# Kernel optimization log

Measured on AMD Instinct MI355X. Metric: run time of the kernel, lower is better.

## Reference

```python
import jax, jax.numpy as jnp
import numpy as np

NEG = -1e6  # SequenceMask fill value from original code


def setup_inputs() -> dict:
    key = jax.random.key(0)
    ks = jax.random.split(key, 7)
    B, Tq, Tk, U = 32, 1024, 1024, 256
    return {
        "query": jax.random.normal(ks[0], (B, Tq, U), dtype=jnp.float32),
        "key": jax.random.normal(ks[1], (B, Tk, U), dtype=jnp.float32),
        "value": jax.random.normal(ks[2], (B, Tk, U), dtype=jnp.float32),
        "valid_length": jax.random.randint(ks[3], (B,), 0, Tk, dtype=jnp.int32),
        "W_k": jax.random.normal(ks[4], (U, U), dtype=jnp.float32) * (1.0 / np.sqrt(U)),
        "W_q": jax.random.normal(ks[5], (U, U), dtype=jnp.float32) * (1.0 / np.sqrt(U)),
        "v": jax.random.normal(ks[6], (U,), dtype=jnp.float32) * (1.0 / np.sqrt(U)),
    }


def reference(query, key, value, valid_length, W_k, W_q, v):
    # Original applies W_k to query and W_q to key (naming swap kept faithfully).
    tq = jnp.tanh(jnp.einsum('bqu,vu->bqv', query, W_k))  # (B,Tq,U)
    tk = jnp.tanh(jnp.einsum('bku,vu->bkv', key, W_q))    # (B,Tk,U)
    # v is linear over (tq_i + tk_j): decompose to avoid (B,Tq,Tk,U) tensor.
    sq = jnp.einsum('bqu,u->bq', tq, v)  # (B,Tq)
    sk = jnp.einsum('bku,u->bk', tk, v)  # (B,Tk)
    scores = sq[:, :, None] + sk[:, None, :]  # (B,Tq,Tk)
    Tk_ = key.shape[1]
    mask = jnp.arange(Tk_)[None, None, :] < valid_length[:, None, None]  # (B,1,Tk)
    scores = jnp.where(mask, scores, NEG)
    attn = jax.nn.softmax(scores, axis=-1)  # dropout p=0 (eval) -> identity
    return jnp.einsum('bqk,bkd->bqd', attn, value)
```

## Files before the change

kernel.cpp:

```cpp
#include <hip/hip_runtime.h>
#include <hip/hip_fp16.h>
#include <math.h>

#define NB 32
#define TQ 1024
#define TK 1024
#define UD 256

typedef __attribute__((ext_vector_type(8))) _Float16 f16x8;
typedef __attribute__((ext_vector_type(4))) _Float16 f16x4;
typedef __attribute__((ext_vector_type(4))) float f32x4;

__device__ __forceinline__ int lds_off(int r, int s) {
  return ((r << 6) + (s << 4)) ^ ((r & 7) << 4);
}

__device__ __forceinline__ float fast_tanh(float x) {
  const float e = __expf(2.0f * x);
  return 1.0f - 2.0f / (e + 1.0f);
}

__global__ __launch_bounds__(256) void cvt_wq_kernel(
    const float* __restrict__ Wq, _Float16* __restrict__ wq16) {
  const int i = (blockIdx.x * 256 + threadIdx.x) * 4;
  const float4 w = *reinterpret_cast<const float4*>(Wq + i);
  f16x4 h;
  h[0] = (_Float16)w.x; h[1] = (_Float16)w.y;
  h[2] = (_Float16)w.z; h[3] = (_Float16)w.w;
  *reinterpret_cast<f16x4*>(wq16 + i) = h;
}

__global__ __launch_bounds__(256) void sk_mfma_kernel(
    const float* __restrict__ key, const _Float16* __restrict__ wq16,
    const float* __restrict__ v, float* __restrict__ sk) {
  __shared__ __align__(16) char lds[2 * 4096];

  const int row0 = blockIdx.x * 64;
  const int tid = threadIdx.x;
  const int lane = tid & 63;
  const int wc = tid >> 6;
  const int lx = lane & 15;
  const int lg = lane >> 4;

  float vv[4];
#pragma unroll
  for (int n = 0; n < 4; ++n) vv[n] = v[wc * 64 + n * 16 + lx];

  f32x4 acc[4][4];
#pragma unroll
  for (int m = 0; m < 4; ++m)
#pragma unroll
    for (int n = 0; n < 4; ++n) acc[m][n] = (f32x4){0.f, 0.f, 0.f, 0.f};

  const int ar = tid >> 2, as = tid & 3;
  const float* gA = &key[(size_t)(row0 + ar) * UD + as * 8];

  const _Float16* gB[4];
#pragma unroll
  for (int n = 0; n < 4; ++n)
    gB[n] = wq16 + (size_t)(wc * 64 + n * 16 + lx) * UD + lg * 8;

  float4 a0 = *reinterpret_cast<const float4*>(gA);
  float4 a1 = *reinterpret_cast<const float4*>(gA + 4);
  f16x8 bfrag[2][4];
#pragma unroll
  for (int n = 0; n < 4; ++n)
    bfrag[0][n] = *reinterpret_cast<const f16x8*>(gB[n]);

#pragma unroll
  for (int kc = 0; kc < 8; ++kc) {
    const int cur = kc & 1;
    f16x8 h;
    h[0] = (_Float16)a0.x; h[1] = (_Float16)a0.y;
    h[2] = (_Float16)a0.z; h[3] = (_Float16)a0.w;
    h[4] = (_Float16)a1.x; h[5] = (_Float16)a1.y;
    h[6] = (_Float16)a1.z; h[7] = (_Float16)a1.w;
    *reinterpret_cast<f16x8*>(lds + cur * 4096 + lds_off(ar, as)) = h;
    if (kc < 7) {
      const int kn = (kc + 1) * 32;
      a0 = *reinterpret_cast<const float4*>(gA + kn);
      a1 = *reinterpret_cast<const float4*>(gA + kn + 4);
#pragma unroll
      for (int n = 0; n < 4; ++n)
        bfrag[(kc + 1) & 1][n] =
            *reinterpret_cast<const f16x8*>(gB[n] + kn);
    }
    __syncthreads();
    f16x8 af[4];
#pragma unroll
    for (int m = 0; m < 4; ++m)
      af[m] = *reinterpret_cast<const f16x8*>(
          lds + cur * 4096 + lds_off(m * 16 + lx, lg));
#pragma unroll
    for (int m = 0; m < 4; ++m)
#pragma unroll
      for (int n = 0; n < 4; ++n)
        acc[m][n] = __builtin_amdgcn_mfma_f32_16x16x32_f16(
            af[m], bfrag[cur][n], acc[m][n], 0, 0, 0);
  }

  float* red = (float*)lds;

  float part[4][4];
#pragma unroll
  for (int m = 0; m < 4; ++m)
#pragma unroll
    for (int r = 0; r < 4; ++r) part[m][r] = 0.f;
#pragma unroll
  for (int m = 0; m < 4; ++m)
#pragma unroll
    for (int n = 0; n < 4; ++n)
#pragma unroll
      for (int r = 0; r < 4; ++r)
        part[m][r] += vv[n] * fast_tanh(acc[m][n][r]);

#pragma unroll
  for (int m = 0; m < 4; ++m)
#pragma unroll
    for (int r = 0; r < 4; ++r) {
      float s = part[m][r];
      s += __shfl_xor(s, 1);
      s += __shfl_xor(s, 2);
      s += __shfl_xor(s, 4);
      s += __shfl_xor(s, 8);
      if (lx == 0) red[(m * 16 + lg * 4 + r) * 4 + wc] = s;
    }
  __syncthreads();
  if (tid < 64) {
    sk[row0 + tid] = red[tid * 4 + 0] + red[tid * 4 + 1] +
                     red[tid * 4 + 2] + red[tid * 4 + 3];
  }
}

__global__ __launch_bounds__(256) void pv_kernel(
    const float* __restrict__ sk, const int* __restrict__ vlen,
    const float* __restrict__ value, float* __restrict__ part) {
  const int b = blockIdx.x >> 4;
  const int ch = blockIdx.x & 15;
  const int tid = threadIdx.x;
  const int vl = vlen[b];
  __shared__ float wbuf[64];
  __shared__ float red4[8];
  __shared__ float racc[1024];
  const float* skb = sk + b * TK;

  if (vl == 0) {
    if (tid < 64) wbuf[tid] = 1.0f / (float)TK;
  } else {
    float m = -1e30f;
#pragma unroll
    for (int idx = 0; idx < 4; ++idx) {
      const int k = tid + idx * 256;
      if (k < vl) m = fmaxf(m, skb[k]);
    }
    for (int off = 1; off < 64; off <<= 1) m = fmaxf(m, __shfl_xor(m, off));
    if ((tid & 63) == 0) red4[tid >> 6] = m;
    __syncthreads();
    m = fmaxf(fmaxf(red4[0], red4[1]), fmaxf(red4[2], red4[3]));
    float zs = 0.f;
#pragma unroll
    for (int idx = 0; idx < 4; ++idx) {
      const int k = tid + idx * 256;
      zs += (k < vl) ? expf(skb[k] - m) : 0.f;
    }
    for (int off = 1; off < 64; off <<= 1) zs += __shfl_xor(zs, off);
    if ((tid & 63) == 0) red4[4 + (tid >> 6)] = zs;
    __syncthreads();
    const float rz = 1.0f / (red4[4] + red4[5] + red4[6] + red4[7]);
    if (tid < 64) {
      const int k = ch * 64 + tid;
      wbuf[tid] = (k < vl) ? expf(skb[k] - m) * rz : 0.f;
    }
  }
  __syncthreads();

  const int ko = tid >> 6;
  const int dl = (tid & 63) * 4;
  const float* vb = value + ((size_t)b * TK + ch * 64) * UD;
  float4 a = make_float4(0.f, 0.f, 0.f, 0.f);
#pragma unroll 4
  for (int kk = ko; kk < 64; kk += 4) {
    const float wk = wbuf[kk];
    const float4 x = *reinterpret_cast<const float4*>(vb + (size_t)kk * UD + dl);
    a.x = fmaf(wk, x.x, a.x);
    a.y = fmaf(wk, x.y, a.y);
    a.z = fmaf(wk, x.z, a.z);
    a.w = fmaf(wk, x.w, a.w);
  }
  *reinterpret_cast<float4*>(&racc[ko * 256 + dl]) = a;
  __syncthreads();
  const float s =
      racc[tid] + racc[256 + tid] + racc[512 + tid] + racc[768 + tid];
  part[(size_t)(b * 16 + ch) * UD + tid] = s;
}

__global__ __launch_bounds__(256) void bcast_kernel(
    const float* __restrict__ part, float* __restrict__ out) {
  const int b = blockIdx.x >> 4;
  const int qc = blockIdx.x & 15;
  const int tid = threadIdx.x;
  const int qoff = tid >> 6;
  const int dd = (tid & 63) * 4;

  float4 s = make_float4(0.f, 0.f, 0.f, 0.f);
#pragma unroll
  for (int c = 0; c < 16; ++c) {
    const float4 p = *reinterpret_cast<const float4*>(
        &part[(size_t)(b * 16 + c) * UD + dd]);
    s.x += p.x; s.y += p.y; s.z += p.z; s.w += p.w;
  }

  float* ob = out + (size_t)b * TQ * UD + (size_t)qc * 64 * UD;
#pragma unroll 4
  for (int q4 = 0; q4 < 16; ++q4) {
    *reinterpret_cast<float4*>(&ob[(size_t)(q4 * 4 + qoff) * UD + dd]) = s;
  }
}

extern "C" void kernel_launch(void* const* d_in, const int* in_sizes, int n_in,
                              void* d_out, int out_size, void* d_ws,
                              size_t ws_size, hipStream_t stream) {
  const float* key = (const float*)d_in[1];
  const float* value = (const float*)d_in[2];
  const int* vlen = (const int*)d_in[3];
  const float* Wq = (const float*)d_in[5];
  const float* v = (const float*)d_in[6];
  float* out = (float*)d_out;

  char* ws = (char*)d_ws;
  _Float16* wq16 = (_Float16*)(ws);
  float* sk = (float*)(ws + 131072);
  float* part = (float*)(ws + 262144);

  cvt_wq_kernel<<<64, 256, 0, stream>>>(Wq, wq16);
  sk_mfma_kernel<<<(NB * TK) / 64, 256, 0, stream>>>(key, wq16, v, sk);
  pv_kernel<<<NB * 16, 256, 0, stream>>>(sk, vlen, value, part);
  bcast_kernel<<<NB * 16, 256, 0, stream>>>(part, out);
}
```

Measured before the change: 50.01 us.

## Stage full W_q in LDS and load key fragments directly per wave

The score kernel now stages the whole fp16 W_q in shared memory, in two 64KB halves pre-laid-out by the conversion kernel in a fragment-friendly order. Each wave loads its key rows straight from global memory into MFMA A fragments, and each wave owns 16 rows across all 256 output columns. This removes the per-k-step key staging through LDS and the cross-wave reduction. The cost is 64KB of LDS per block, which limits occupancy, and every block re-reads all of W_q. The softmax exp calls are also switched to fast __expf.

```diff
diff --git a/kernel.cpp b/kernel.cpp
--- a/kernel.cpp
+++ b/kernel.cpp
@@ -8,12 +8,7 @@
 #define UD 256
 
 typedef __attribute__((ext_vector_type(8))) _Float16 f16x8;
-typedef __attribute__((ext_vector_type(4))) _Float16 f16x4;
 typedef __attribute__((ext_vector_type(4))) float f32x4;
-
-__device__ __forceinline__ int lds_off(int r, int s) {
-  return ((r << 6) + (s << 4)) ^ ((r & 7) << 4);
-}
 
 __device__ __forceinline__ float fast_tanh(float x) {
   const float e = __expf(2.0f * x);
@@ -21,114 +16,84 @@
 }
 
 __global__ __launch_bounds__(256) void cvt_wq_kernel(
-    const float* __restrict__ Wq, _Float16* __restrict__ wq16) {
-  const int i = (blockIdx.x * 256 + threadIdx.x) * 4;
-  const float4 w = *reinterpret_cast<const float4*>(Wq + i);
-  f16x4 h;
-  h[0] = (_Float16)w.x; h[1] = (_Float16)w.y;
-  h[2] = (_Float16)w.z; h[3] = (_Float16)w.w;
-  *reinterpret_cast<f16x4*>(wq16 + i) = h;
-}
-
-__global__ __launch_bounds__(256) void sk_mfma_kernel(
-    const float* __restrict__ key, const _Float16* __restrict__ wq16,
+    const float* __restrict__ Wq, _Float16* __restrict__ wq16t) {
+  const int idx = blockIdx.x * 256 + threadIdx.x;
+  const int u = idx >> 5;
+  const int ks = idx & 31;
+  const float4 w0 = *reinterpret_cast<const float4*>(Wq + u * UD + ks * 8);
+  const float4 w1 = *reinterpret_cast<const float4*>(Wq + u * UD + ks * 8 + 4);
+  f16x8 h;
+  h[0] = (_Float16)w0.x; h[1] = (_Float16)w0.y;
+  h[2] = (_Float16)w0.z; h[3] = (_Float16)w0.w;
+  h[4] = (_Float16)w1.x; h[5] = (_Float16)w1.y;
+  h[6] = (_Float16)w1.z; h[7] = (_Float16)w1.w;
+  *reinterpret_cast<f16x8*>(wq16t + ((size_t)ks * 256 + u) * 8) = h;
+}
+
+__global__ __launch_bounds__(256, 2) void sk_mfma_kernel(
+    const float* __restrict__ key, const _Float16* __restrict__ wq16t,
     const float* __restrict__ v, float* __restrict__ sk) {
-  __shared__ __align__(16) char lds[2 * 4096];
-
-  const int row0 = blockIdx.x * 64;
+  __shared__ _Float16 Bt[32768];
+
   const int tid = threadIdx.x;
   const int lane = tid & 63;
   const int wc = tid >> 6;
   const int lx = lane & 15;
   const int lg = lane >> 4;
-
-  float vv[4];
-#pragma unroll
-  for (int n = 0; n < 4; ++n) vv[n] = v[wc * 64 + n * 16 + lx];
-
-  f32x4 acc[4][4];
-#pragma unroll
-  for (int m = 0; m < 4; ++m)
-#pragma unroll
-    for (int n = 0; n < 4; ++n) acc[m][n] = (f32x4){0.f, 0.f, 0.f, 0.f};
-
-  const int ar = tid >> 2, as = tid & 3;
-  const float* gA = &key[(size_t)(row0 + ar) * UD + as * 8];
-
-  const _Float16* gB[4];
-#pragma unroll
-  for (int n = 0; n < 4; ++n)
-    gB[n] = wq16 + (size_t)(wc * 64 + n * 16 + lx) * UD + lg * 8;
-
-  float4 a0 = *reinterpret_cast<const float4*>(gA);
-  float4 a1 = *reinterpret_cast<const float4*>(gA + 4);
-  f16x8 bfrag[2][4];
-#pragma unroll
-  for (int n = 0; n < 4; ++n)
-    bfrag[0][n] = *reinterpret_cast<const f16x8*>(gB[n]);
-
-#pragma unroll
-  for (int kc = 0; kc < 8; ++kc) {
-    const int cur = kc & 1;
-    f16x8 h;
-    h[0] = (_Float16)a0.x; h[1] = (_Float16)a0.y;
-    h[2] = (_Float16)a0.z; h[3] = (_Float16)a0.w;
-    h[4] = (_Float16)a1.x; h[5] = (_Float16)a1.y;
-    h[6] = (_Float16)a1.z; h[7] = (_Float16)a1.w;
-    *reinterpret_cast<f16x8*>(lds + cur * 4096 + lds_off(ar, as)) = h;
-    if (kc < 7) {
-      const int kn = (kc + 1) * 32;
-      a0 = *reinterpret_cast<const float4*>(gA + kn);
-      a1 = *reinterpret_cast<const float4*>(gA + kn + 4);
-#pragma unroll
-      for (int n = 0; n < 4; ++n)
-        bfrag[(kc + 1) & 1][n] =
-            *reinterpret_cast<const f16x8*>(gB[n] + kn);
-    }
-    __syncthreads();
-    f16x8 af[4];
-#pragma unroll
-    for (int m = 0; m < 4; ++m)
-      af[m] = *reinterpret_cast<const f16x8*>(
-          lds + cur * 4096 + lds_off(m * 16 + lx, lg));
-#pragma unroll
-    for (int m = 0; m < 4; ++m)
-#pragma unroll
-      for (int n = 0; n < 4; ++n)
-        acc[m][n] = __builtin_amdgcn_mfma_f32_16x16x32_f16(
-            af[m], bfrag[cur][n], acc[m][n], 0, 0, 0);
-  }
-
-  float* red = (float*)lds;
-
-  float part[4][4];
-#pragma unroll
-  for (int m = 0; m < 4; ++m)
-#pragma unroll
-    for (int r = 0; r < 4; ++r) part[m][r] = 0.f;
-#pragma unroll
-  for (int m = 0; m < 4; ++m)
-#pragma unroll
-    for (int n = 0; n < 4; ++n)
-#pragma unroll
-      for (int r = 0; r < 4; ++r)
-        part[m][r] += vv[n] * fast_tanh(acc[m][n][r]);
-
-#pragma unroll
-  for (int m = 0; m < 4; ++m)
-#pragma unroll
-    for (int r = 0; r < 4; ++r) {
-      float s = part[m][r];
-      s += __shfl_xor(s, 1);
-      s += __shfl_xor(s, 2);
-      s += __shfl_xor(s, 4);
-      s += __shfl_xor(s, 8);
-      if (lx == 0) red[(m * 16 + lg * 4 + r) * 4 + wc] = s;
-    }
-  __syncthreads();
-  if (tid < 64) {
-    sk[row0 + tid] = red[tid * 4 + 0] + red[tid * 4 + 1] +
-                     red[tid * 4 + 2] + red[tid * 4 + 3];
+  const int arow = blockIdx.x * 64 + wc * 16 + lx;
+  const float* gA = key + (size_t)arow * UD + lg * 8;
+
+  f32x4 acc[16];
+#pragma unroll
+  for (int n = 0; n < 16; ++n) acc[n] = (f32x4){0.f, 0.f, 0.f, 0.f};
+
+#pragma unroll
+  for (int p = 0; p < 2; ++p) {
+    {
+      const f16x8* src =
+          reinterpret_cast<const f16x8*>(wq16t + (size_t)p * 32768) + tid;
+      f16x8* dst = reinterpret_cast<f16x8*>(Bt) + tid;
+#pragma unroll
+      for (int it = 0; it < 16; ++it) dst[it * 256] = src[it * 256];
+    }
+    __syncthreads();
+
+#pragma unroll
+    for (int kc = 0; kc < 4; ++kc) {
+      const int k0 = p * 128 + kc * 32;
+      const float4 a0 = *reinterpret_cast<const float4*>(gA + k0);
+      const float4 a1 = *reinterpret_cast<const float4*>(gA + k0 + 4);
+      f16x8 af;
+      af[0] = (_Float16)a0.x; af[1] = (_Float16)a0.y;
+      af[2] = (_Float16)a0.z; af[3] = (_Float16)a0.w;
+      af[4] = (_Float16)a1.x; af[5] = (_Float16)a1.y;
+      af[6] = (_Float16)a1.z; af[7] = (_Float16)a1.w;
+#pragma unroll
+      for (int n = 0; n < 16; ++n) {
+        const f16x8 bf = *reinterpret_cast<const f16x8*>(
+            Bt + (((kc * 4 + lg) * 256) + n * 16 + lx) * 8);
+        acc[n] =
+            __builtin_amdgcn_mfma_f32_16x16x32_f16(af, bf, acc[n], 0, 0, 0);
+      }
+    }
+    __syncthreads();
+  }
+
+  float out_r[4] = {0.f, 0.f, 0.f, 0.f};
+#pragma unroll
+  for (int n = 0; n < 16; ++n) {
+    const float vn = v[n * 16 + lx];
+#pragma unroll
+    for (int r = 0; r < 4; ++r) out_r[r] += vn * fast_tanh(acc[n][r]);
+  }
+#pragma unroll
+  for (int r = 0; r < 4; ++r) {
+    float s = out_r[r];
+    s += __shfl_xor(s, 1);
+    s += __shfl_xor(s, 2);
+    s += __shfl_xor(s, 4);
+    s += __shfl_xor(s, 8);
+    if (lx == 0) sk[blockIdx.x * 64 + wc * 16 + lg * 4 + r] = s;
   }
 }
 
@@ -161,7 +126,7 @@
 #pragma unroll
     for (int idx = 0; idx < 4; ++idx) {
       const int k = tid + idx * 256;
-      zs += (k < vl) ? expf(skb[k] - m) : 0.f;
+      zs += (k < vl) ? __expf(skb[k] - m) : 0.f;
     }
     for (int off = 1; off < 64; off <<= 1) zs += __shfl_xor(zs, off);
     if ((tid & 63) == 0) red4[4 + (tid >> 6)] = zs;
@@ -169,7 +134,7 @@
     const float rz = 1.0f / (red4[4] + red4[5] + red4[6] + red4[7]);
     if (tid < 64) {
       const int k = ch * 64 + tid;
-      wbuf[tid] = (k < vl) ? expf(skb[k] - m) * rz : 0.f;
+      wbuf[tid] = (k < vl) ? __expf(skb[k] - m) * rz : 0.f;
     }
   }
   __syncthreads();
@@ -181,7 +146,8 @@
 #pragma unroll 4
   for (int kk = ko; kk < 64; kk += 4) {
     const float wk = wbuf[kk];
-    const float4 x = *reinterpret_cast<const float4*>(vb + (size_t)kk * UD + dl);
+    const float4 x =
+        *reinterpret_cast<const float4*>(vb + (size_t)kk * UD + dl);
     a.x = fmaf(wk, x.x, a.x);
     a.y = fmaf(wk, x.y, a.y);
     a.z = fmaf(wk, x.z, a.z);
@@ -228,12 +194,12 @@
   float* out = (float*)d_out;
 
   char* ws = (char*)d_ws;
-  _Float16* wq16 = (_Float16*)(ws);
+  _Float16* wq16t = (_Float16*)(ws);
   float* sk = (float*)(ws + 131072);
   float* part = (float*)(ws + 262144);
 
-  cvt_wq_kernel<<<64, 256, 0, stream>>>(Wq, wq16);
-  sk_mfma_kernel<<<(NB * TK) / 64, 256, 0, stream>>>(key, wq16, v, sk);
+  cvt_wq_kernel<<<32, 256, 0, stream>>>(Wq, wq16t);
+  sk_mfma_kernel<<<(NB * TK) / 64, 256, 0, stream>>>(key, wq16t, v, sk);
   pv_kernel<<<NB * 16, 256, 0, stream>>>(sk, vlen, value, part);
   bcast_kernel<<<NB * 16, 256, 0, stream>>>(part, out);
 }
```

Measured after the change: 48.79 us. 2.4% less time.
